# Kernel optimization log

Measured on AMD Instinct MI355X. Metric: run time of the kernel, lower is better.

The kernel has to match this reference:

```python
import jax, jax.numpy as jnp
from jax import lax
import numpy as np

B, CIN, COUT, H, W, K = 4, 64, 64, 128, 128, 3
FACTOR = 2.0  # ivcf, tile != first-layer override path -> factor = ivcf
DN = ('NCHW', 'OIHW', 'NCHW')


def cimu_conv2d(x, weight, bias, factor):
    """Bit-serial int8 conv emulation: 8 bit-plane convs, per-plane clamp/round."""
    xq = jnp.clip(x, -128, 127).astype(jnp.int8).astype(jnp.uint8)  # two's complement bits
    shifts = jnp.arange(8, dtype=jnp.uint8).reshape(8, 1, 1, 1, 1)
    bits = ((xq[None] >> shifts) & jnp.uint8(1)).astype(jnp.float32)  # (8,B,C,Hp,Wp)
    P, b, c, hp, wp = bits.shape
    y = lax.conv_general_dilated(bits.reshape(P * b, c, hp, wp), weight,
                                 window_strides=(1, 1), padding='VALID',
                                 dimension_numbers=DN)  # (8B, Cout, Ho, Wo)
    y = y.reshape(P, b, y.shape[1], y.shape[2], y.shape[3])
    y = jnp.clip(jnp.round(y / factor), -128, 127)
    y = jnp.round(jnp.round(y * factor))
    plane_w = jnp.array([1., 2., 4., 8., 16., 32., 64., -128.], dtype=jnp.float32)
    y = jnp.einsum('pbchw,p->bchw', y, plane_w)
    return y + bias.reshape(1, -1, 1, 1)


def setup_inputs() -> dict:
    key = jax.random.key(0)
    ks = jax.random.split(key, 8)
    ri = lambda k, shape, lo, hi: (jax.random.randint(k, shape, lo, hi)).astype(jnp.float32)
    return {
        'cast_in':   ri(ks[0], (B, CIN, H, W), -128, 128),
        'merge_in':  ri(ks[1], (B, COUT, H, W), -128, 128),
        'gather_in': ri(ks[2], (B, COUT, H, W), -128, 128),
        'conv_weight': ri(ks[3], (COUT, CIN, K, K), -3, 4),
        'conv_bias':   ri(ks[4], (COUT,), -8, 8),
        'ctrans_i': ri(ks[5], (COUT,), 1, 4),            # per-channel integer multiplier
        'ctrans_s': jnp.full((COUT,), -1.0, jnp.float32),  # per-channel shift exponent
        'strans_i': jnp.float32(3.0),
        'strans_s': jnp.float32(-2.0),
        'atrans_i': jnp.float32(1.0),
        'atrans_s': jnp.float32(0.0),
    }


def reference(cast_in, merge_in, gather_in, conv_weight, conv_bias,
              ctrans_i, ctrans_s, strans_i, strans_s, atrans_i, atrans_s):
    # conv_pads = [1,1,1,1] (left,right,top,bottom on last two dims)
    x = jnp.pad(cast_in, ((0, 0), (0, 0), (1, 1), (1, 1)))
    x = cimu_conv2d(x, conv_weight, conv_bias, FACTOR)
    # merge add
    x = x + merge_in
    # merge-node quantize (hardtrans): mult = ctrans_i / 2^{-ctrans_s}
    cmult = (ctrans_i / (2.0 ** (-ctrans_s))).reshape(1, -1, 1, 1)
    x = jnp.clip(jnp.round(x * cmult), -128, 127)
    # gather add + quantize
    x = x + gather_in
    smult = strans_i / (2.0 ** (-strans_s))
    x = jnp.clip(jnp.round(x * smult), -128, 127)
    # Relu + quantize
    x = jax.nn.relu(x)
    amult = atrans_i / (2.0 ** (-atrans_s))
    x = jnp.clip(jnp.round(x * amult), -128, 127)
    # pool_pads = [0,0,0,0] (no-op), MaxPool 2x2 stride 2
    x = lax.reduce_window(x, -jnp.inf, lax.max, (1, 1, 2, 2), (1, 1, 2, 2), 'VALID')
    return x
```

## Files before the change

### kernel.cpp

```cpp
#include <hip/hip_runtime.h>
#include <cstdint>


typedef int i32x4  __attribute__((ext_vector_type(4)));
typedef int i32x16 __attribute__((ext_vector_type(16)));

#define XB_OFF   0u
#define XB_BYTES 4326400u
#define WPK_OFF  XB_BYTES
#define WPK_BYTES 36864u

__global__ __launch_bounds__(256) void k_stage(const float* __restrict__ s_cast,
                                               const float* __restrict__ wsrc,
                                               uint8_t* __restrict__ ws) {
  const int blk = blockIdx.x, t = threadIdx.x;
  if (blk >= 656) {
    const int hb = blk - 656;
    const int b = hb >> 1, r = (hb & 1) ? 129 : 0;
    uint8_t* base = ws + XB_OFF + ((size_t)(b * 130 + r) * 130) * 64;
    const uint4 z = {0, 0, 0, 0};
#pragma unroll
    for (int i = 0; i < 3; ++i) {
      const int s = i * 256 + t;
      if (s < 520) *(uint4*)(base + (size_t)s * 16) = z;
    }
    return;
  }
  if (blk >= 512) {
    const int idx = (blk - 512) * 256 + t;
    const int i = idx & 15, l = (idx >> 4) & 63, gg = (idx >> 10) & 1,
              c = idx >> 11;
    const int k = c * 32 + (l >> 5) * 16 + i;
    const int tap = k >> 6, ci = k & 63;
    const int kh = tap / 3, kw = tap % 3;
    const int cco = gg * 32 + (l & 31);
    const float wv = wsrc[((cco * 64 + ci) * 3 + kh) * 3 + kw];
    ((int8_t*)(ws + WPK_OFF))[idx] = (int8_t)(int)wv;
    return;
  }
  const int b = blk >> 7, h = blk & 127;
  __shared__ uint8_t lds[128 * 68];
  const float* s0 = s_cast + ((size_t)(b * 64) * 128 + h) * 128;
#pragma unroll
  for (int ci0 = 0; ci0 < 64; ci0 += 2) {
    const int ci = ci0 + (t >> 7), w = t & 127;
    const float v = s0[ci * 16384 + w];
    lds[w * 68 + ci] = (uint8_t)((int)v & 0xFF);
  }
  __syncthreads();
  uint8_t* row = ws + XB_OFF + (((size_t)b * 130 + h + 1) * 130) * 64;
#pragma unroll
  for (int j = 0; j < 8; ++j) {
    const int f = j * 256 + t;
    const int w = f >> 4, ci4 = f & 15;
    const uint32_t val = *(const uint32_t*)&lds[w * 68 + ci4 * 4];
    *(uint32_t*)(row + 64 + (size_t)f * 4) = val;
  }
  if (t < 8) {
    const int col = (t < 4) ? 0 : 129, seg = t & 3;
    const uint4 z = {0, 0, 0, 0};
    *(uint4*)(row + (size_t)col * 64 + seg * 16) = z;
  }
}

__global__ __launch_bounds__(256, 2) void k_main(
    const unsigned char* __restrict__ xb, const float* __restrict__ mgf,
    const float* __restrict__ gtf, const int8_t* __restrict__ wpk,
    const float* __restrict__ bias, const float* __restrict__ cti,
    const float* __restrict__ cts, const float* __restrict__ sti,
    const float* __restrict__ sts, const float* __restrict__ ati,
    const float* __restrict__ ats, float* __restrict__ outp) {
  const int tid = threadIdx.x, lane = tid & 63, wv = tid >> 6;
  const int blk = blockIdx.x;
  const int wq = blk & 3, ho = (blk >> 2) & 63, b = blk >> 8;
  const int h = ho * 2, w0 = wq * 32;

  __shared__ uint4 ldsx4[640];
  __shared__ i32x4 wpkl[2304];
  __shared__ uint8_t mgt8[2][2][64][36];
  __shared__ float po_lds[16 * 64];
  uint8_t* ldsx = (uint8_t*)ldsx4;

  {
    const unsigned char* xrow = xb + ((size_t)(b * 130 + h) * 130 + w0) * 64;
#pragma unroll
    for (int i = 0; i < 3; ++i) {
      const int s = i * 256 + tid;
      if (s < 640) {
        const int row = s / 160, rm = s - row * 160;
        const int col = rm >> 2, ci16 = rm & 3;
        const int gcol = col < 34 ? col : 33;
        const uint4 v =
            *(const uint4*)(xrow + ((size_t)row * 130 + gcol) * 64 + ci16 * 16);
        *(uint4*)(ldsx + (row * 40 + col) * 64 + ci16 * 16) = v;
      }
    }
  }

#pragma unroll
  for (int i = 0; i < 9; ++i) {
    const int s = i * 256 + tid;
    wpkl[s] = *(const i32x4*)(wpk + (size_t)s * 16);
  }

#pragma unroll
  for (int which = 0; which < 2; ++which) {
    const float* sp = which ? gtf : mgf;
#pragma unroll
    for (int i = 0; i < 4; ++i) {
      const int slot = i * 256 + tid;
      const int co = slot >> 4, r = slot & 15, hh = r & 1, seg = r >> 1;
      const float4 v = *(const float4*)(
          sp + ((size_t)((b * 64 + co) * 128 + h + hh)) * 128 + w0 + seg * 4);
      const uint32_t pk =
          ((uint32_t)((int)v.x & 0xFF)) | ((uint32_t)((int)v.y & 0xFF) << 8) |
          ((uint32_t)((int)v.z & 0xFF) << 16) | ((uint32_t)((int)v.w & 0xFF) << 24);
      *(uint32_t*)&mgt8[which][hh][co][seg * 4] = pk;
    }
  }

  const int pix = (lane & 31) >> 3;
  const int plane = lane & 7;
  const int khalf = lane >> 5;
  const int dh = pix >> 1, dw = pix & 1;
  const uint8_t* lbw =
      ldsx + (dh * 40 + dw) * 64 + khalf * 16 + wv * 512;

  const int col = lane & 31;
  const float bs0 = bias[col], bs1 = bias[col + 32];
  const float cm0 = ldexpf(cti[col], (int)cts[col]);
  const float cm1 = ldexpf(cti[col + 32], (int)cts[col + 32]);
  const float sm = ldexpf(sti[0], (int)sts[0]);
  const float am = ldexpf(ati[0], (int)ats[0]);
  float pwl[4];
  pwl[0] = khalf ? 16.f : 1.f;
  pwl[1] = khalf ? 32.f : 2.f;
  pwl[2] = khalf ? 64.f : 4.f;
  pwl[3] = khalf ? -128.f : 8.f;

  __syncthreads();

#define XOFF(c) ((((c) >> 1) / 3) * 2560 + (((c) >> 1) % 3) * 64 + ((c)&1) * 32)
  i32x16 acc[4][2] = {};
#pragma unroll
  for (int c = 0; c < 18; ++c) {
    const i32x4 B0 = wpkl[(c * 2 + 0) * 64 + lane];
    const i32x4 B1 = wpkl[(c * 2 + 1) * 64 + lane];
#pragma unroll
    for (int q = 0; q < 4; ++q) {
      const uint4 vv = *(const uint4*)(lbw + q * 128 + XOFF(c));
      i32x4 av;
      av[0] = (int)((vv.x >> plane) & 0x01010101u);
      av[1] = (int)((vv.y >> plane) & 0x01010101u);
      av[2] = (int)((vv.z >> plane) & 0x01010101u);
      av[3] = (int)((vv.w >> plane) & 0x01010101u);
      acc[q][0] = __builtin_amdgcn_mfma_i32_32x32x32_i8(av, B0, acc[q][0], 0, 0, 0);
      acc[q][1] = __builtin_amdgcn_mfma_i32_32x32x32_i8(av, B1, acc[q][1], 0, 0, 0);
    }
  }
#undef XOFF

#pragma unroll
  for (int q = 0; q < 4; ++q) {
    const int wol = wv * 4 + q;
#pragma unroll
    for (int gg = 0; gg < 2; ++gg) {
      const float bs = gg ? bs1 : bs0;
      const float cm = gg ? cm1 : cm0;
      const int cc = gg * 32 + col;
      float psum[4];
#pragma unroll
      for (int px = 0; px < 4; ++px) {
        float s = 0.f;
#pragma unroll
        for (int j = 0; j < 4; ++j) {
          const float y = (float)acc[q][gg][px * 4 + j];
          const float qq = fminf(fmaxf(rintf(y * 0.5f), -128.f), 127.f);
          s = fmaf(pwl[j], 2.f * qq, s);
        }
        psum[px] = s;
      }
#pragma unroll
      for (int px = 0; px < 4; ++px)
        psum[px] += __shfl_xor(psum[px], 32);

      float po = -3.0e38f;
#pragma unroll
      for (int px = 0; px < 4; ++px) {
        const int ww = wol * 2 + (px & 1);
        const float mgv = (float)(int)(signed char)mgt8[0][px >> 1][cc][ww];
        const float gtv = (float)(int)(signed char)mgt8[1][px >> 1][cc][ww];
        const float x1 = psum[px] + bs + mgv;
        const float x2 = fminf(fmaxf(rintf(x1 * cm), -128.f), 127.f);
        const float x3 = x2 + gtv;
        const float x4 = fminf(fmaxf(rintf(x3 * sm), -128.f), 127.f);
        const float x5 = fmaxf(x4, 0.f);
        const float x6 = fminf(fmaxf(rintf(x5 * am), -128.f), 127.f);
        po = fmaxf(po, x6);
      }
      if (lane < 32)
        po_lds[wol * 64 + gg * 32 + col] = po;
    }
  }

  __syncthreads();
  {
    const int tco = tid >> 2, seg = tid & 3;
    float4 v;
    v.x = po_lds[(seg * 4 + 0) * 64 + tco];
    v.y = po_lds[(seg * 4 + 1) * 64 + tco];
    v.z = po_lds[(seg * 4 + 2) * 64 + tco];
    v.w = po_lds[(seg * 4 + 3) * 64 + tco];
    float* dst = outp + (((size_t)(b * 64 + tco)) * 64 + ho) * 64 + wq * 16 + seg * 4;
    *(float4*)dst = v;
  }
}

extern "C" void kernel_launch(void* const* d_in, const int* in_sizes, int n_in,
                              void* d_out, int out_size, void* d_ws, size_t ws_size,
                              hipStream_t stream) {
  const float* cast_in = (const float*)d_in[0];
  const float* merge_in = (const float*)d_in[1];
  const float* gather_in = (const float*)d_in[2];
  const float* conv_w = (const float*)d_in[3];
  const float* conv_b = (const float*)d_in[4];
  const float* cti = (const float*)d_in[5];
  const float* cts = (const float*)d_in[6];
  const float* sti = (const float*)d_in[7];
  const float* sts = (const float*)d_in[8];
  const float* ati = (const float*)d_in[9];
  const float* ats = (const float*)d_in[10];

  uint8_t* ws = (uint8_t*)d_ws;
  uint8_t* xb = ws + XB_OFF;
  int8_t* wpk = (int8_t*)(ws + WPK_OFF);

  k_stage<<<664, 256, 0, stream>>>(cast_in, conv_w, ws);
  k_main<<<1024, 256, 0, stream>>>(xb, merge_in, gather_in, wpk, conv_b, cti,
                                   cts, sti, sts, ati, ats, (float*)d_out);
}
```

Measured before the change: 35.63 us.

## Process two pooled output rows per block and XOR-swizzle weight LDS layout

Each block now computes two pooled output rows (four conv rows), so the 36KB packed weight tile and the input halo rows are loaded into LDS once per two rows instead of once per row. This halves the grid to 512 blocks and enlarges the LDS footprint. The weight LDS writes and reads also use an XOR swizzle on the lane index, intended to reduce bank conflicts on the B-operand loads. The risks are lower occupancy from the extra LDS, fewer blocks than CUs times two on a 256-CU part, and more serialized work per block.

```diff
diff --git a/kernel.cpp b/kernel.cpp
--- a/kernel.cpp
+++ b/kernel.cpp
@@ -72,26 +72,25 @@
     const float* __restrict__ ats, float* __restrict__ outp) {
   const int tid = threadIdx.x, lane = tid & 63, wv = tid >> 6;
   const int blk = blockIdx.x;
-  const int wq = blk & 3, ho = (blk >> 2) & 63, b = blk >> 8;
-  const int h = ho * 2, w0 = wq * 32;
-
-  __shared__ uint4 ldsx4[640];
+  const int wq = blk & 3, hp = (blk >> 2) & 31, b = blk >> 7;
+  const int h0 = hp * 4, w0 = wq * 32;
+
+  __shared__ uint4 ldsx4[960];
   __shared__ i32x4 wpkl[2304];
-  __shared__ uint8_t mgt8[2][2][64][36];
-  __shared__ float po_lds[16 * 64];
+  __shared__ uint8_t mgt8[2][4][64][36];
+  __shared__ float po_lds[2][16][64];
   uint8_t* ldsx = (uint8_t*)ldsx4;
 
   {
-    const unsigned char* xrow = xb + ((size_t)(b * 130 + h) * 130 + w0) * 64;
-#pragma unroll
-    for (int i = 0; i < 3; ++i) {
+#pragma unroll
+    for (int i = 0; i < 4; ++i) {
       const int s = i * 256 + tid;
-      if (s < 640) {
+      if (s < 960) {
         const int row = s / 160, rm = s - row * 160;
         const int col = rm >> 2, ci16 = rm & 3;
         const int gcol = col < 34 ? col : 33;
-        const uint4 v =
-            *(const uint4*)(xrow + ((size_t)row * 130 + gcol) * 64 + ci16 * 16);
+        const uint4 v = *(const uint4*)(
+            xb + ((size_t)((b * 130 + h0 + row) * 130) + w0 + gcol) * 64 + ci16 * 16);
         *(uint4*)(ldsx + (row * 40 + col) * 64 + ci16 * 16) = v;
       }
     }
@@ -100,18 +99,19 @@
 #pragma unroll
   for (int i = 0; i < 9; ++i) {
     const int s = i * 256 + tid;
-    wpkl[s] = *(const i32x4*)(wpk + (size_t)s * 16);
+    const int sw = (s & ~63) | ((s & 63) ^ ((s >> 3) & 7));
+    wpkl[sw] = *(const i32x4*)(wpk + (size_t)s * 16);
   }
 
 #pragma unroll
   for (int which = 0; which < 2; ++which) {
     const float* sp = which ? gtf : mgf;
 #pragma unroll
-    for (int i = 0; i < 4; ++i) {
+    for (int i = 0; i < 8; ++i) {
       const int slot = i * 256 + tid;
-      const int co = slot >> 4, r = slot & 15, hh = r & 1, seg = r >> 1;
+      const int co = slot >> 5, r5 = slot & 31, hh = r5 >> 3, seg = r5 & 7;
       const float4 v = *(const float4*)(
-          sp + ((size_t)((b * 64 + co) * 128 + h + hh)) * 128 + w0 + seg * 4);
+          sp + ((size_t)((b * 64 + co) * 128 + h0 + hh)) * 128 + w0 + seg * 4);
       const uint32_t pk =
           ((uint32_t)((int)v.x & 0xFF)) | ((uint32_t)((int)v.y & 0xFF) << 8) |
           ((uint32_t)((int)v.z & 0xFF) << 16) | ((uint32_t)((int)v.w & 0xFF) << 24);
@@ -123,8 +123,7 @@
   const int plane = lane & 7;
   const int khalf = lane >> 5;
   const int dh = pix >> 1, dw = pix & 1;
-  const uint8_t* lbw =
-      ldsx + (dh * 40 + dw) * 64 + khalf * 16 + wv * 512;
+  const int lsw = lane ^ ((lane >> 3) & 7);
 
   const int col = lane & 31;
   const float bs0 = bias[col], bs1 = bias[col + 32];
@@ -141,78 +140,89 @@
   __syncthreads();
 
 #define XOFF(c) ((((c) >> 1) / 3) * 2560 + (((c) >> 1) % 3) * 64 + ((c)&1) * 32)
-  i32x16 acc[4][2] = {};
-#pragma unroll
-  for (int c = 0; c < 18; ++c) {
-    const i32x4 B0 = wpkl[(c * 2 + 0) * 64 + lane];
-    const i32x4 B1 = wpkl[(c * 2 + 1) * 64 + lane];
+#pragma unroll
+  for (int r = 0; r < 2; ++r) {
+    const uint8_t* lbw =
+        ldsx + ((dh + 2 * r) * 40 + dw) * 64 + khalf * 16 + wv * 512;
+
+    i32x16 acc[4][2] = {};
+#pragma unroll
+    for (int c = 0; c < 18; ++c) {
+      const i32x4 B0 = wpkl[(c * 2 + 0) * 64 + lsw];
+      const i32x4 B1 = wpkl[(c * 2 + 1) * 64 + lsw];
+#pragma unroll
+      for (int q = 0; q < 4; ++q) {
+        const uint4 vv = *(const uint4*)(lbw + q * 128 + XOFF(c));
+        i32x4 av;
+        av[0] = (int)((vv.x >> plane) & 0x01010101u);
+        av[1] = (int)((vv.y >> plane) & 0x01010101u);
+        av[2] = (int)((vv.z >> plane) & 0x01010101u);
+        av[3] = (int)((vv.w >> plane) & 0x01010101u);
+        acc[q][0] = __builtin_amdgcn_mfma_i32_32x32x32_i8(av, B0, acc[q][0], 0, 0, 0);
+        acc[q][1] = __builtin_amdgcn_mfma_i32_32x32x32_i8(av, B1, acc[q][1], 0, 0, 0);
+      }
+    }
+
 #pragma unroll
     for (int q = 0; q < 4; ++q) {
-      const uint4 vv = *(const uint4*)(lbw + q * 128 + XOFF(c));
-      i32x4 av;
-      av[0] = (int)((vv.x >> plane) & 0x01010101u);
-      av[1] = (int)((vv.y >> plane) & 0x01010101u);
-      av[2] = (int)((vv.z >> plane) & 0x01010101u);
-      av[3] = (int)((vv.w >> plane) & 0x01010101u);
-      acc[q][0] = __builtin_amdgcn_mfma_i32_32x32x32_i8(av, B0, acc[q][0], 0, 0, 0);
-      acc[q][1] = __builtin_amdgcn_mfma_i32_32x32x32_i8(av, B1, acc[q][1], 0, 0, 0);
+      const int wol = wv * 4 + q;
+#pragma unroll
+      for (int gg = 0; gg < 2; ++gg) {
+        const float bs = gg ? bs1 : bs0;
+        const float cm = gg ? cm1 : cm0;
+        const int cc = gg * 32 + col;
+        float psum[4];
+#pragma unroll
+        for (int px = 0; px < 4; ++px) {
+          float s = 0.f;
+#pragma unroll
+          for (int j = 0; j < 4; ++j) {
+            const float y = (float)acc[q][gg][px * 4 + j];
+            const float qq = fminf(fmaxf(rintf(y * 0.5f), -128.f), 127.f);
+            s = fmaf(pwl[j], 2.f * qq, s);
+          }
+          psum[px] = s;
+        }
+#pragma unroll
+        for (int px = 0; px < 4; ++px)
+          psum[px] += __shfl_xor(psum[px], 32);
+
+        float po = -3.0e38f;
+#pragma unroll
+        for (int px = 0; px < 4; ++px) {
+          const int ww = wol * 2 + (px & 1);
+          const int hh = 2 * r + (px >> 1);
+          const float mgv = (float)(int)(signed char)mgt8[0][hh][cc][ww];
+          const float gtv = (float)(int)(signed char)mgt8[1][hh][cc][ww];
+          const float x1 = psum[px] + bs + mgv;
+          const float x2 = fminf(fmaxf(rintf(x1 * cm), -128.f), 127.f);
+          const float x3 = x2 + gtv;
+          const float x4 = fminf(fmaxf(rintf(x3 * sm), -128.f), 127.f);
+          const float x5 = fmaxf(x4, 0.f);
+          const float x6 = fminf(fmaxf(rintf(x5 * am), -128.f), 127.f);
+          po = fmaxf(po, x6);
+        }
+        if (lane < 32)
+          po_lds[r][wol][gg * 32 + col] = po;
+      }
     }
   }
 #undef XOFF
-
-#pragma unroll
-  for (int q = 0; q < 4; ++q) {
-    const int wol = wv * 4 + q;
-#pragma unroll
-    for (int gg = 0; gg < 2; ++gg) {
-      const float bs = gg ? bs1 : bs0;
-      const float cm = gg ? cm1 : cm0;
-      const int cc = gg * 32 + col;
-      float psum[4];
-#pragma unroll
-      for (int px = 0; px < 4; ++px) {
-        float s = 0.f;
-#pragma unroll
-        for (int j = 0; j < 4; ++j) {
-          const float y = (float)acc[q][gg][px * 4 + j];
-          const float qq = fminf(fmaxf(rintf(y * 0.5f), -128.f), 127.f);
-          s = fmaf(pwl[j], 2.f * qq, s);
-        }
-        psum[px] = s;
-      }
-#pragma unroll
-      for (int px = 0; px < 4; ++px)
-        psum[px] += __shfl_xor(psum[px], 32);
-
-      float po = -3.0e38f;
-#pragma unroll
-      for (int px = 0; px < 4; ++px) {
-        const int ww = wol * 2 + (px & 1);
-        const float mgv = (float)(int)(signed char)mgt8[0][px >> 1][cc][ww];
-        const float gtv = (float)(int)(signed char)mgt8[1][px >> 1][cc][ww];
-        const float x1 = psum[px] + bs + mgv;
-        const float x2 = fminf(fmaxf(rintf(x1 * cm), -128.f), 127.f);
-        const float x3 = x2 + gtv;
-        const float x4 = fminf(fmaxf(rintf(x3 * sm), -128.f), 127.f);
-        const float x5 = fmaxf(x4, 0.f);
-        const float x6 = fminf(fmaxf(rintf(x5 * am), -128.f), 127.f);
-        po = fmaxf(po, x6);
-      }
-      if (lane < 32)
-        po_lds[wol * 64 + gg * 32 + col] = po;
-    }
-  }
 
   __syncthreads();
   {
     const int tco = tid >> 2, seg = tid & 3;
-    float4 v;
-    v.x = po_lds[(seg * 4 + 0) * 64 + tco];
-    v.y = po_lds[(seg * 4 + 1) * 64 + tco];
-    v.z = po_lds[(seg * 4 + 2) * 64 + tco];
-    v.w = po_lds[(seg * 4 + 3) * 64 + tco];
-    float* dst = outp + (((size_t)(b * 64 + tco)) * 64 + ho) * 64 + wq * 16 + seg * 4;
-    *(float4*)dst = v;
+#pragma unroll
+    for (int r = 0; r < 2; ++r) {
+      float4 v;
+      v.x = po_lds[r][seg * 4 + 0][tco];
+      v.y = po_lds[r][seg * 4 + 1][tco];
+      v.z = po_lds[r][seg * 4 + 2][tco];
+      v.w = po_lds[r][seg * 4 + 3][tco];
+      float* dst = outp + (((size_t)(b * 64 + tco)) * 64 + hp * 2 + r) * 64 +
+                   wq * 16 + seg * 4;
+      *(float4*)dst = v;
+    }
   }
 }
 
@@ -236,6 +246,6 @@
   int8_t* wpk = (int8_t*)(ws + WPK_OFF);
 
   k_stage<<<664, 256, 0, stream>>>(cast_in, conv_w, ws);
-  k_main<<<1024, 256, 0, stream>>>(xb, merge_in, gather_in, wpk, conv_b, cti,
-                                   cts, sti, sts, ati, ats, (float*)d_out);
+  k_main<<<512, 256, 0, stream>>>(xb, merge_in, gather_in, wpk, conv_b, cti,
+                                  cts, sti, sts, ati, ats, (float*)d_out);
 }
```

Result: slower. 36.55 us (+2.6%).

## Halve per-block output tile width and double grid for higher occupancy

Applied to the files above, without the earlier changes.

Each k_main block now covers 16 input columns (8 pooled outputs) instead of 32, so the grid doubles to 2048 blocks and each wave runs 2 accumulator tiles instead of 4. This cuts accumulator registers and LDS per block, and launch bounds are raised to 3 blocks per CU for more latency hiding. The cost is that every block still stages the full packed weight matrix into LDS, so weight traffic doubles. Input halo overlap between blocks also grows, and output stores shrink from float4 to float2.

```diff
diff --git a/kernel.cpp b/kernel.cpp
--- a/kernel.cpp
+++ b/kernel.cpp
@@ -63,37 +63,32 @@
   }
 }
 
-__global__ __launch_bounds__(256, 2) void k_main(
+__global__ __launch_bounds__(256, 3) void k_main(
     const unsigned char* __restrict__ xb, const float* __restrict__ mgf,
     const float* __restrict__ gtf, const int8_t* __restrict__ wpk,
     const float* __restrict__ bias, const float* __restrict__ cti,
     const float* __restrict__ cts, const float* __restrict__ sti,
     const float* __restrict__ sts, const float* __restrict__ ati,
     const float* __restrict__ ats, float* __restrict__ outp) {
-  const int tid = threadIdx.x, lane = tid & 63, wv = tid >> 6;
+  const int tid = threadIdx.x, lane = tid & 63, wg = tid >> 6;
   const int blk = blockIdx.x;
-  const int wq = blk & 3, ho = (blk >> 2) & 63, b = blk >> 8;
-  const int h = ho * 2, w0 = wq * 32;
-
-  __shared__ uint4 ldsx4[640];
+  const int wq = blk & 7, ho = (blk >> 3) & 63, b = blk >> 9;
+  const int h0 = ho * 2, w0 = wq * 16;
+
+  __shared__ uint8_t ldsx[4 * 20 * 64];
   __shared__ i32x4 wpkl[2304];
-  __shared__ uint8_t mgt8[2][2][64][36];
-  __shared__ float po_lds[16 * 64];
-  uint8_t* ldsx = (uint8_t*)ldsx4;
-
-  {
-    const unsigned char* xrow = xb + ((size_t)(b * 130 + h) * 130 + w0) * 64;
-#pragma unroll
-    for (int i = 0; i < 3; ++i) {
-      const int s = i * 256 + tid;
-      if (s < 640) {
-        const int row = s / 160, rm = s - row * 160;
-        const int col = rm >> 2, ci16 = rm & 3;
-        const int gcol = col < 34 ? col : 33;
-        const uint4 v =
-            *(const uint4*)(xrow + ((size_t)row * 130 + gcol) * 64 + ci16 * 16);
-        *(uint4*)(ldsx + (row * 40 + col) * 64 + ci16 * 16) = v;
-      }
+  __shared__ uint8_t mgt8[2][2][64][20];
+  __shared__ float po_lds[8][65];
+
+#pragma unroll
+  for (int i = 0; i < 2; ++i) {
+    const int s = i * 256 + tid;
+    if (s < 288) {
+      const int row = s / 72, rm = s - row * 72;
+      const int col = rm >> 2, ci16 = rm & 3;
+      const uint4 v = *(const uint4*)(
+          xb + ((size_t)((b * 130 + h0 + row) * 130) + w0 + col) * 64 + ci16 * 16);
+      *(uint4*)(ldsx + (row * 20 + col) * 64 + ci16 * 16) = v;
     }
   }
 
@@ -107,11 +102,11 @@
   for (int which = 0; which < 2; ++which) {
     const float* sp = which ? gtf : mgf;
 #pragma unroll
-    for (int i = 0; i < 4; ++i) {
+    for (int i = 0; i < 2; ++i) {
       const int slot = i * 256 + tid;
-      const int co = slot >> 4, r = slot & 15, hh = r & 1, seg = r >> 1;
+      const int co = slot >> 3, r3 = slot & 7, hh = r3 >> 2, seg = r3 & 3;
       const float4 v = *(const float4*)(
-          sp + ((size_t)((b * 64 + co) * 128 + h + hh)) * 128 + w0 + seg * 4);
+          sp + ((size_t)((b * 64 + co) * 128 + h0 + hh)) * 128 + w0 + seg * 4);
       const uint32_t pk =
           ((uint32_t)((int)v.x & 0xFF)) | ((uint32_t)((int)v.y & 0xFF) << 8) |
           ((uint32_t)((int)v.z & 0xFF) << 16) | ((uint32_t)((int)v.w & 0xFF) << 24);
@@ -123,8 +118,7 @@
   const int plane = lane & 7;
   const int khalf = lane >> 5;
   const int dh = pix >> 1, dw = pix & 1;
-  const uint8_t* lbw =
-      ldsx + (dh * 40 + dw) * 64 + khalf * 16 + wv * 512;
+  const uint8_t* lbw = ldsx + ((dh * 20) + (wg * 4 + dw)) * 64 + khalf * 16;
 
   const int col = lane & 31;
   const float bs0 = bias[col], bs1 = bias[col + 32];
@@ -140,14 +134,14 @@
 
   __syncthreads();
 
-#define XOFF(c) ((((c) >> 1) / 3) * 2560 + (((c) >> 1) % 3) * 64 + ((c)&1) * 32)
-  i32x16 acc[4][2] = {};
+#define XOFF(c) ((((c) >> 1) / 3) * 1280 + (((c) >> 1) % 3) * 64 + ((c)&1) * 32)
+  i32x16 acc[2][2] = {};
 #pragma unroll
   for (int c = 0; c < 18; ++c) {
     const i32x4 B0 = wpkl[(c * 2 + 0) * 64 + lane];
     const i32x4 B1 = wpkl[(c * 2 + 1) * 64 + lane];
 #pragma unroll
-    for (int q = 0; q < 4; ++q) {
+    for (int q = 0; q < 2; ++q) {
       const uint4 vv = *(const uint4*)(lbw + q * 128 + XOFF(c));
       i32x4 av;
       av[0] = (int)((vv.x >> plane) & 0x01010101u);
@@ -161,8 +155,8 @@
 #undef XOFF
 
 #pragma unroll
-  for (int q = 0; q < 4; ++q) {
-    const int wol = wv * 4 + q;
+  for (int q = 0; q < 2; ++q) {
+    const int wol = wg * 2 + q;
 #pragma unroll
     for (int gg = 0; gg < 2; ++gg) {
       const float bs = gg ? bs1 : bs0;
@@ -188,8 +182,9 @@
 #pragma unroll
       for (int px = 0; px < 4; ++px) {
         const int ww = wol * 2 + (px & 1);
-        const float mgv = (float)(int)(signed char)mgt8[0][px >> 1][cc][ww];
-        const float gtv = (float)(int)(signed char)mgt8[1][px >> 1][cc][ww];
+        const int hh = px >> 1;
+        const float mgv = (float)(int)(signed char)mgt8[0][hh][cc][ww];
+        const float gtv = (float)(int)(signed char)mgt8[1][hh][cc][ww];
         const float x1 = psum[px] + bs + mgv;
         const float x2 = fminf(fmaxf(rintf(x1 * cm), -128.f), 127.f);
         const float x3 = x2 + gtv;
@@ -199,20 +194,18 @@
         po = fmaxf(po, x6);
       }
       if (lane < 32)
-        po_lds[wol * 64 + gg * 32 + col] = po;
+        po_lds[wol][cc] = po;
     }
   }
 
   __syncthreads();
   {
     const int tco = tid >> 2, seg = tid & 3;
-    float4 v;
-    v.x = po_lds[(seg * 4 + 0) * 64 + tco];
-    v.y = po_lds[(seg * 4 + 1) * 64 + tco];
-    v.z = po_lds[(seg * 4 + 2) * 64 + tco];
-    v.w = po_lds[(seg * 4 + 3) * 64 + tco];
-    float* dst = outp + (((size_t)(b * 64 + tco)) * 64 + ho) * 64 + wq * 16 + seg * 4;
-    *(float4*)dst = v;
+    float2 v;
+    v.x = po_lds[seg * 2 + 0][tco];
+    v.y = po_lds[seg * 2 + 1][tco];
+    float* dst = outp + (((size_t)(b * 64 + tco)) * 64 + ho) * 64 + wq * 8 + seg * 2;
+    *(float2*)dst = v;
   }
 }
 
@@ -236,6 +229,6 @@
   int8_t* wpk = (int8_t*)(ws + WPK_OFF);
 
   k_stage<<<664, 256, 0, stream>>>(cast_in, conv_w, ws);
-  k_main<<<1024, 256, 0, stream>>>(xb, merge_in, gather_in, wpk, conv_b, cti,
+  k_main<<<2048, 256, 0, stream>>>(xb, merge_in, gather_in, wpk, conv_b, cti,
                                    cts, sti, sts, ati, ats, (float*)d_out);
 }
```

Measured after the change: 35.93 us. Within noise of the previous version (+0.8%).
